# Kernel optimization log

Hardware: AMD Instinct MI355X
Metric: run time of the kernel (lower is better)

Reference implementation:

```python
import jax, jax.numpy as jnp
import numpy as np

B, T, D, H = 2048, 2048, 3, 32  # batch, time steps, input_size, hidden_size


def setup_inputs() -> dict:
    key = jax.random.key(0)
    k0, k1, k2, k3, k4 = jax.random.split(key, 5)
    lim = 1.0 / np.sqrt(H)  # eqx.nn.GRUCell init range
    inp = jax.random.normal(k0, (B, T, D), dtype=jnp.float32)
    weight_ih = jax.random.uniform(k1, (3 * H, D), minval=-lim, maxval=lim, dtype=jnp.float32)
    weight_hh = jax.random.uniform(k2, (3 * H, H), minval=-lim, maxval=lim, dtype=jnp.float32)
    bias = jax.random.uniform(k3, (3 * H,), minval=-lim, maxval=lim, dtype=jnp.float32)
    bias_n = jax.random.uniform(k4, (H,), minval=-lim, maxval=lim, dtype=jnp.float32)
    return {"inp": inp, "weight_ih": weight_ih, "weight_hh": weight_hh,
            "bias": bias, "bias_n": bias_n}


def reference(inp, weight_ih, weight_hh, bias, bias_n):
    # inp: [B, T, D]. Faithful batched version of PinnWithGRU.__call__:
    # scan an eqx.nn.GRUCell over time from a zero hidden state, output hidden[0] per step.
    b = inp.shape[0]
    h0 = jnp.zeros((b, H), dtype=inp.dtype)
    xs = jnp.swapaxes(inp, 0, 1)  # [T, B, D]

    def step(h, x):
        ig = x @ weight_ih.T + bias      # [B, 3H] input gates (+ bias, as in eqx)
        hg = h @ weight_hh.T             # [B, 3H] hidden gates
        ir, iz, ia = jnp.split(ig, 3, axis=-1)
        hr, hz, ha = jnp.split(hg, 3, axis=-1)
        r = jax.nn.sigmoid(ir + hr)
        z = jax.nn.sigmoid(iz + hz)
        n = jnp.tanh(ia + bias_n + r * ha)
        h_new = (1.0 - z) * n + z * h
        return h_new, h_new[:, 0]        # emit first hidden unit per step

    _, out = jax.lax.scan(step, h0, xs)  # out: [T, B]
    return jnp.swapaxes(out, 0, 1)[..., None]  # [B, T, 1] (matches per-seq [T, 1])
```

## Files before the change

### kernel.cpp

```cpp
#include <hip/hip_runtime.h>


#define GRU_B 2048
#define GRU_T 2048
#define GRU_D 3
#define GRU_H 32
#define CHUNK 32
#define XPAD 104

typedef unsigned int uint2v __attribute__((ext_vector_type(2)));

__device__ __forceinline__ float fast_sigmoid(float x) {
    float e = __expf(-x);
    return __builtin_amdgcn_rcpf(1.0f + e);
}
__device__ __forceinline__ float fast_tanh(float x) {
    float e = __expf(2.0f * x);
    return 1.0f - 2.0f * __builtin_amdgcn_rcpf(e + 1.0f);
}

#define DPPF(v, CTRL) __int_as_float(__builtin_amdgcn_update_dpp( \
    0, __float_as_int(v), (CTRL), 0xF, 0xF, false))

template<bool SEL>
__device__ __forceinline__ float swap32(float v) {
    uint2v r = __builtin_amdgcn_permlane32_swap(
        __float_as_uint(v), __float_as_uint(v), false, false);
    return __uint_as_float(SEL ? r.x : r.y);
}

template<bool SEL>
__device__ void gru_fast(
    const float* __restrict__ xp, float* __restrict__ ob,
    const float* __restrict__ w_ih, const float* __restrict__ w_hh,
    const float* __restrict__ bias, const float* __restrict__ bias_n,
    float* __restrict__ x_lds, int lane, int hf, int p, int dir)
{
    const int li = lane & 15;
    const int bb = 16 * (lane >> 5);

    float wrO[16], wrX[16], wzO[16], wzX[16], wnO[16], wnX[16];
#pragma unroll
    for (int j = 0; j < 16; ++j) {
        const int kk = (li + dir * j + 16) & 15;
        const int kown = bb + kk;
        const int koth = (bb ^ 16) + kk;
        wrO[j] = w_hh[(size_t)p * GRU_H + kown];
        wrX[j] = w_hh[(size_t)p * GRU_H + koth];
        wzO[j] = w_hh[(size_t)(GRU_H + p) * GRU_H + kown];
        wzX[j] = w_hh[(size_t)(GRU_H + p) * GRU_H + koth];
        wnO[j] = w_hh[(size_t)(2 * GRU_H + p) * GRU_H + kown];
        wnX[j] = w_hh[(size_t)(2 * GRU_H + p) * GRU_H + koth];
    }
    float wir[GRU_D], wiz[GRU_D], win[GRU_D];
#pragma unroll
    for (int d = 0; d < GRU_D; ++d) {
        wir[d] = w_ih[(size_t)p * GRU_D + d];
        wiz[d] = w_ih[(size_t)(GRU_H + p) * GRU_D + d];
        win[d] = w_ih[(size_t)(2 * GRU_H + p) * GRU_D + d];
    }
    const float bR = bias[p];
    const float bZ = bias[GRU_H + p];
    const float bN = bias[2 * GRU_H + p] + bias_n[p];

    float* xw = x_lds + XPAD * hf;
    const float* xr = x_lds + XPAD * hf;

    float h = 0.0f;
    float xa = xp[p], xb = xp[32 + p], xc = xp[64 + p];

    for (int c = 0; c < GRU_T / CHUNK; ++c) {
        xw[p] = xa; xw[32 + p] = xb; xw[64 + p] = xc;
        if (c + 1 < GRU_T / CHUNK) {
            const size_t nb = (size_t)(c + 1) * (CHUNK * GRU_D);
            xa = xp[nb + p]; xb = xp[nb + 32 + p]; xc = xp[nb + 64 + p];
        }
        float x0c = xr[0], x1c = xr[1], x2c = xr[2];
        float outreg = 0.0f;

#pragma unroll 8
        for (int s = 0; s < CHUNK; ++s) {
            const float aR = fmaf(wir[2], x2c, fmaf(wir[1], x1c, fmaf(wir[0], x0c, bR)));
            const float aZ = fmaf(wiz[2], x2c, fmaf(wiz[1], x1c, fmaf(wiz[0], x0c, bZ)));
            const float aN = fmaf(win[2], x2c, fmaf(win[1], x1c, fmaf(win[0], x0c, bN)));

            float x0n = x0c, x1n = x1c, x2n = x2c;
            if (s + 1 < CHUNK) {
                x0n = xr[3 * (s + 1) + 0];
                x1n = xr[3 * (s + 1) + 1];
                x2n = xr[3 * (s + 1) + 2];
            }

            const float hsw = swap32<SEL>(h);
            float hr_[16], ho_[16];
            hr_[0] = h;    ho_[0] = hsw;
            hr_[1]  = DPPF(h, 0x121);   ho_[1]  = DPPF(hsw, 0x121);
            hr_[2]  = DPPF(h, 0x122);   ho_[2]  = DPPF(hsw, 0x122);
            hr_[3]  = DPPF(h, 0x123);   ho_[3]  = DPPF(hsw, 0x123);
            hr_[4]  = DPPF(h, 0x124);   ho_[4]  = DPPF(hsw, 0x124);
            hr_[5]  = DPPF(h, 0x125);   ho_[5]  = DPPF(hsw, 0x125);
            hr_[6]  = DPPF(h, 0x126);   ho_[6]  = DPPF(hsw, 0x126);
            hr_[7]  = DPPF(h, 0x127);   ho_[7]  = DPPF(hsw, 0x127);
            hr_[8]  = DPPF(h, 0x128);   ho_[8]  = DPPF(hsw, 0x128);
            hr_[9]  = DPPF(h, 0x129);   ho_[9]  = DPPF(hsw, 0x129);
            hr_[10] = DPPF(h, 0x12A);   ho_[10] = DPPF(hsw, 0x12A);
            hr_[11] = DPPF(h, 0x12B);   ho_[11] = DPPF(hsw, 0x12B);
            hr_[12] = DPPF(h, 0x12C);   ho_[12] = DPPF(hsw, 0x12C);
            hr_[13] = DPPF(h, 0x12D);   ho_[13] = DPPF(hsw, 0x12D);
            hr_[14] = DPPF(h, 0x12E);   ho_[14] = DPPF(hsw, 0x12E);
            hr_[15] = DPPF(h, 0x12F);   ho_[15] = DPPF(hsw, 0x12F);

            float rO0 = aR, rO1 = 0.f, rX0 = 0.f, rX1 = 0.f;
            float zO0 = aZ, zO1 = 0.f, zX0 = 0.f, zX1 = 0.f;
            float nO0 = 0.f, nO1 = 0.f, nX0 = 0.f, nX1 = 0.f;
#pragma unroll
            for (int j = 0; j < 8; ++j) {
                rO0 = fmaf(wrO[j],     hr_[j],     rO0);
                rO1 = fmaf(wrO[j + 8], hr_[j + 8], rO1);
                rX0 = fmaf(wrX[j],     ho_[j],     rX0);
                rX1 = fmaf(wrX[j + 8], ho_[j + 8], rX1);
                zO0 = fmaf(wzO[j],     hr_[j],     zO0);
                zO1 = fmaf(wzO[j + 8], hr_[j + 8], zO1);
                zX0 = fmaf(wzX[j],     ho_[j],     zX0);
                zX1 = fmaf(wzX[j + 8], ho_[j + 8], zX1);
                nO0 = fmaf(wnO[j],     hr_[j],     nO0);
                nO1 = fmaf(wnO[j + 8], hr_[j + 8], nO1);
                nX0 = fmaf(wnX[j],     ho_[j],     nX0);
                nX1 = fmaf(wnX[j + 8], ho_[j + 8], nX1);
            }
            const float rs = (rO0 + rO1) + (rX0 + rX1);
            const float zs = (zO0 + zO1) + (zX0 + zX1);
            const float ns = (nO0 + nO1) + (nX0 + nX1);

            const float rg = fast_sigmoid(rs);
            const float zg = fast_sigmoid(zs);
            const float ng = fast_tanh(fmaf(rg, ns, aN));
            h = fmaf(zg, h - ng, ng);

            const float h0A = __uint_as_float(
                (unsigned)__builtin_amdgcn_readfirstlane(__float_as_int(h)));
            const float h0B = __uint_as_float(
                (unsigned)__builtin_amdgcn_readlane(__float_as_int(h), 16));
            const float want = hf ? h0B : h0A;
            if (p == s) outreg = want;

            x0c = x0n; x1c = x1n; x2c = x2n;
        }
        ob[c * CHUNK + p] = outreg;
    }
}

__device__ void gru_lds(
    const float* __restrict__ xp, float* __restrict__ ob,
    const float* __restrict__ w_ih, const float* __restrict__ w_hh,
    const float* __restrict__ bias, const float* __restrict__ bias_n,
    float* __restrict__ x_lds, float* __restrict__ out_stage,
    float* __restrict__ h2, int lane, int hf, int p)
{
    float wr[32], wz[32], wn[32];
#pragma unroll
    for (int k = 0; k < 32; ++k) {
        wr[k] = w_hh[(size_t)p * GRU_H + k];
        wz[k] = w_hh[(size_t)(GRU_H + p) * GRU_H + k];
        wn[k] = w_hh[(size_t)(2 * GRU_H + p) * GRU_H + k];
    }
    float wir[GRU_D], wiz[GRU_D], win[GRU_D];
#pragma unroll
    for (int d = 0; d < GRU_D; ++d) {
        wir[d] = w_ih[(size_t)p * GRU_D + d];
        wiz[d] = w_ih[(size_t)(GRU_H + p) * GRU_D + d];
        win[d] = w_ih[(size_t)(2 * GRU_H + p) * GRU_D + d];
    }
    const float bR = bias[p];
    const float bZ = bias[GRU_H + p];
    const float bN = bias[2 * GRU_H + p] + bias_n[p];

    float* hw = h2 + 48 * hf + p;
    const float4* hv = (const float4*)(h2 + 48 * hf);
    float* xw = x_lds + XPAD * hf;
    const float* xr = x_lds + XPAD * hf;
    float* osw = out_stage + 32 * hf;
    const bool cap = (lane & 47) == 0;

    float h = 0.0f;
    *hw = 0.0f;
    float xa = xp[p], xb = xp[32 + p], xc = xp[64 + p];

    for (int c = 0; c < GRU_T / CHUNK; ++c) {
        xw[p] = xa; xw[32 + p] = xb; xw[64 + p] = xc;
        if (c + 1 < GRU_T / CHUNK) {
            const size_t nb = (size_t)(c + 1) * (CHUNK * GRU_D);
            xa = xp[nb + p]; xb = xp[nb + 32 + p]; xc = xp[nb + 64 + p];
        }
#pragma unroll 8
        for (int s = 0; s < CHUNK; ++s) {
            const float x0 = xr[3 * s + 0];
            const float x1 = xr[3 * s + 1];
            const float x2 = xr[3 * s + 2];
            float4 hk[8];
#pragma unroll
            for (int q = 0; q < 8; ++q) hk[q] = hv[q];

            const float aR = fmaf(wir[2], x2, fmaf(wir[1], x1, fmaf(wir[0], x0, bR)));
            const float aZ = fmaf(wiz[2], x2, fmaf(wiz[1], x1, fmaf(wiz[0], x0, bZ)));
            const float aN = fmaf(win[2], x2, fmaf(win[1], x1, fmaf(win[0], x0, bN)));

            float r0 = aR, r1 = 0.f, z0 = aZ, z1 = 0.f, n0 = 0.f, n1 = 0.f;
#pragma unroll
            for (int q = 0; q < 8; ++q) {
                const float4 v = hk[q];
                r0 = fmaf(wr[4*q+0], v.x, r0); r1 = fmaf(wr[4*q+1], v.y, r1);
                r0 = fmaf(wr[4*q+2], v.z, r0); r1 = fmaf(wr[4*q+3], v.w, r1);
                z0 = fmaf(wz[4*q+0], v.x, z0); z1 = fmaf(wz[4*q+1], v.y, z1);
                z0 = fmaf(wz[4*q+2], v.z, z0); z1 = fmaf(wz[4*q+3], v.w, z1);
                n0 = fmaf(wn[4*q+0], v.x, n0); n1 = fmaf(wn[4*q+1], v.y, n1);
                n0 = fmaf(wn[4*q+2], v.z, n0); n1 = fmaf(wn[4*q+3], v.w, n1);
            }
            const float rg = fast_sigmoid(r0 + r1);
            const float zg = fast_sigmoid(z0 + z1);
            const float ng = fast_tanh(fmaf(rg, n0 + n1, aN));
            h = fmaf(zg, h - ng, ng);
            if (cap) osw[s] = h;
            *hw = h;
        }
        const float ov = osw[p];
        ob[c * CHUNK + p] = ov;
    }
}

__global__ __launch_bounds__(64, 1) void gru_scan_kernel(
    const float* __restrict__ inp, const float* __restrict__ w_ih,
    const float* __restrict__ w_hh, const float* __restrict__ bias,
    const float* __restrict__ bias_n, float* __restrict__ out)
{
    __shared__ __align__(16) float x_lds[2 * XPAD];
    __shared__ __align__(16) float out_stage[2 * CHUNK];
    __shared__ __align__(16) float h2[80];

    const int lane = threadIdx.x;
    const int hf   = (lane >> 4) & 1;
    const int p    = (lane & 15) + 16 * (lane >> 5);
    const size_t seq = 2 * (size_t)blockIdx.x + hf;

    const float* xp = inp + seq * (size_t)(GRU_T * GRU_D);
    float*       ob = out + seq * (size_t)GRU_T;

    int dir = 0;
    bool swapok = false, sel = false;
    {
        const int li = lane & 15;
        const int d1 = __builtin_amdgcn_update_dpp(0, li, 0x121, 0xF, 0xF, false);
        if (__ballot(d1 == ((li + 1) & 15)) == ~0ULL)       dir = 1;
        else if (__ballot(d1 == ((li + 15) & 15)) == ~0ULL) dir = -1;

        const unsigned ul = (unsigned)lane;
        uint2v q = __builtin_amdgcn_permlane32_swap(ul, ul, false, false);
        const unsigned want = ul ^ 32u;
        const bool okA = __ballot(q.x == want) == ~0ULL;
        const bool okB = __ballot(q.y == want) == ~0ULL;
        swapok = okA || okB;
        sel = okA;
    }

    if (dir != 0 && swapok) {
        if (sel) gru_fast<true >(xp, ob, w_ih, w_hh, bias, bias_n,
                                 x_lds, lane, hf, p, dir);
        else     gru_fast<false>(xp, ob, w_ih, w_hh, bias, bias_n,
                                 x_lds, lane, hf, p, dir);
    } else {
        gru_lds(xp, ob, w_ih, w_hh, bias, bias_n,
                x_lds, out_stage, h2, lane, hf, p);
    }
}

extern "C" void kernel_launch(void* const* d_in, const int* in_sizes, int n_in,
                              void* d_out, int out_size, void* d_ws, size_t ws_size,
                              hipStream_t stream) {
    const float* inp    = (const float*)d_in[0];
    const float* w_ih   = (const float*)d_in[1];
    const float* w_hh   = (const float*)d_in[2];
    const float* bias   = (const float*)d_in[3];
    const float* bias_n = (const float*)d_in[4];
    float* out = (float*)d_out;

    dim3 grid(GRU_B / 2);
    dim3 block(64);
    gru_scan_kernel<<<grid, block, 0, stream>>>(inp, w_ih, w_hh, bias, bias_n, out);
}
```

Baseline: 601.2 us.

## Fuse DPP rotations into fmac instructions and re-layout hidden state exchange

Replaces the separate DPP row-rotate moves plus FMA loop with inline-asm v_fmac_f32_dpp chains, so each rotation is folded into the multiply-accumulate. It also changes how hidden state is distributed across lanes: after each step, the upper half-wave's copy of h is exchanged via permlane16_swap (or ds_bpermute as a fallback), and the previous-state value is selected per lane. This aims to cut instruction count and latency on the serial recurrence critical path. The trade-offs are that each accumulator is now a single serial dependency chain instead of several independent partial sums, and an extra cross-lane exchange is added per step.

After: 616.9 us. 2.6% more time.

```diff
diff --git a/kernel.cpp b/kernel.cpp
--- a/kernel.cpp
+++ b/kernel.cpp
@@ -18,9 +18,9 @@
     float e = __expf(2.0f * x);
     return 1.0f - 2.0f * __builtin_amdgcn_rcpf(e + 1.0f);
 }
-
-#define DPPF(v, CTRL) __int_as_float(__builtin_amdgcn_update_dpp( \
-    0, __float_as_int(v), (CTRL), 0xF, 0xF, false))
+__device__ __forceinline__ float bperm(float v, int baddr) {
+    return __int_as_float(__builtin_amdgcn_ds_bpermute(baddr, __float_as_int(v)));
+}
 
 template<bool SEL>
 __device__ __forceinline__ float swap32(float v) {
@@ -29,12 +29,43 @@
     return __uint_as_float(SEL ? r.x : r.y);
 }
 
-template<bool SEL>
+#if __has_builtin(__builtin_amdgcn_permlane16_swap)
+#define HAVE_P16 1
+#else
+#define HAVE_P16 0
+#endif
+
+#define DOT16(ACC, HSRC, W) \
+  asm("s_nop 1\n\t" \
+      "v_fmac_f32 %0, %1, %2\n\t" \
+      "v_fmac_f32_dpp %0, %1, %3 row_ror:1 row_mask:0xf bank_mask:0xf\n\t" \
+      "v_fmac_f32_dpp %0, %1, %4 row_ror:2 row_mask:0xf bank_mask:0xf\n\t" \
+      "v_fmac_f32_dpp %0, %1, %5 row_ror:3 row_mask:0xf bank_mask:0xf\n\t" \
+      "v_fmac_f32_dpp %0, %1, %6 row_ror:4 row_mask:0xf bank_mask:0xf\n\t" \
+      "v_fmac_f32_dpp %0, %1, %7 row_ror:5 row_mask:0xf bank_mask:0xf\n\t" \
+      "v_fmac_f32_dpp %0, %1, %8 row_ror:6 row_mask:0xf bank_mask:0xf\n\t" \
+      "v_fmac_f32_dpp %0, %1, %9 row_ror:7 row_mask:0xf bank_mask:0xf\n\t" \
+      "v_fmac_f32_dpp %0, %1, %10 row_ror:8 row_mask:0xf bank_mask:0xf\n\t" \
+      "v_fmac_f32_dpp %0, %1, %11 row_ror:9 row_mask:0xf bank_mask:0xf\n\t" \
+      "v_fmac_f32_dpp %0, %1, %12 row_ror:10 row_mask:0xf bank_mask:0xf\n\t" \
+      "v_fmac_f32_dpp %0, %1, %13 row_ror:11 row_mask:0xf bank_mask:0xf\n\t" \
+      "v_fmac_f32_dpp %0, %1, %14 row_ror:12 row_mask:0xf bank_mask:0xf\n\t" \
+      "v_fmac_f32_dpp %0, %1, %15 row_ror:13 row_mask:0xf bank_mask:0xf\n\t" \
+      "v_fmac_f32_dpp %0, %1, %16 row_ror:14 row_mask:0xf bank_mask:0xf\n\t" \
+      "v_fmac_f32_dpp %0, %1, %17 row_ror:15 row_mask:0xf bank_mask:0xf" \
+      : "+v"(ACC) \
+      : "v"(HSRC), "v"((W)[0]), "v"((W)[1]), "v"((W)[2]), "v"((W)[3]), \
+        "v"((W)[4]), "v"((W)[5]), "v"((W)[6]), "v"((W)[7]), "v"((W)[8]), \
+        "v"((W)[9]), "v"((W)[10]), "v"((W)[11]), "v"((W)[12]), "v"((W)[13]), \
+        "v"((W)[14]), "v"((W)[15]))
+
+template<bool SEL32, bool USE16>
 __device__ void gru_fast(
     const float* __restrict__ xp, float* __restrict__ ob,
     const float* __restrict__ w_ih, const float* __restrict__ w_hh,
     const float* __restrict__ bias, const float* __restrict__ bias_n,
-    float* __restrict__ x_lds, int lane, int hf, int p, int dir)
+    float* __restrict__ x_lds, int lane, int hf, int p, int dir,
+    bool sel16, int a16)
 {
     const int li = lane & 15;
     const int bb = 16 * (lane >> 5);
@@ -91,58 +122,48 @@
                 x2n = xr[3 * (s + 1) + 2];
             }
 
-            const float hsw = swap32<SEL>(h);
-            float hr_[16], ho_[16];
-            hr_[0] = h;    ho_[0] = hsw;
-            hr_[1]  = DPPF(h, 0x121);   ho_[1]  = DPPF(hsw, 0x121);
-            hr_[2]  = DPPF(h, 0x122);   ho_[2]  = DPPF(hsw, 0x122);
-            hr_[3]  = DPPF(h, 0x123);   ho_[3]  = DPPF(hsw, 0x123);
-            hr_[4]  = DPPF(h, 0x124);   ho_[4]  = DPPF(hsw, 0x124);
-            hr_[5]  = DPPF(h, 0x125);   ho_[5]  = DPPF(hsw, 0x125);
-            hr_[6]  = DPPF(h, 0x126);   ho_[6]  = DPPF(hsw, 0x126);
-            hr_[7]  = DPPF(h, 0x127);   ho_[7]  = DPPF(hsw, 0x127);
-            hr_[8]  = DPPF(h, 0x128);   ho_[8]  = DPPF(hsw, 0x128);
-            hr_[9]  = DPPF(h, 0x129);   ho_[9]  = DPPF(hsw, 0x129);
-            hr_[10] = DPPF(h, 0x12A);   ho_[10] = DPPF(hsw, 0x12A);
-            hr_[11] = DPPF(h, 0x12B);   ho_[11] = DPPF(hsw, 0x12B);
-            hr_[12] = DPPF(h, 0x12C);   ho_[12] = DPPF(hsw, 0x12C);
-            hr_[13] = DPPF(h, 0x12D);   ho_[13] = DPPF(hsw, 0x12D);
-            hr_[14] = DPPF(h, 0x12E);   ho_[14] = DPPF(hsw, 0x12E);
-            hr_[15] = DPPF(h, 0x12F);   ho_[15] = DPPF(hsw, 0x12F);
-
-            float rO0 = aR, rO1 = 0.f, rX0 = 0.f, rX1 = 0.f;
-            float zO0 = aZ, zO1 = 0.f, zX0 = 0.f, zX1 = 0.f;
-            float nO0 = 0.f, nO1 = 0.f, nX0 = 0.f, nX1 = 0.f;
-#pragma unroll
-            for (int j = 0; j < 8; ++j) {
-                rO0 = fmaf(wrO[j],     hr_[j],     rO0);
-                rO1 = fmaf(wrO[j + 8], hr_[j + 8], rO1);
-                rX0 = fmaf(wrX[j],     ho_[j],     rX0);
-                rX1 = fmaf(wrX[j + 8], ho_[j + 8], rX1);
-                zO0 = fmaf(wzO[j],     hr_[j],     zO0);
-                zO1 = fmaf(wzO[j + 8], hr_[j + 8], zO1);
-                zX0 = fmaf(wzX[j],     ho_[j],     zX0);
-                zX1 = fmaf(wzX[j + 8], ho_[j + 8], zX1);
-                nO0 = fmaf(wnO[j],     hr_[j],     nO0);
-                nO1 = fmaf(wnO[j + 8], hr_[j + 8], nO1);
-                nX0 = fmaf(wnX[j],     ho_[j],     nX0);
-                nX1 = fmaf(wnX[j + 8], ho_[j + 8], nX1);
-            }
-            const float rs = (rO0 + rO1) + (rX0 + rX1);
-            const float zs = (zO0 + zO1) + (zX0 + zX1);
-            const float ns = (nO0 + nO1) + (nX0 + nX1);
+            const float hsw = swap32<SEL32>(h);
+            const float hprev = (lane & 32) ? hsw : h;
+
+            float accOr = aR,  accXr = 0.0f;
+            float accOz = aZ,  accXz = 0.0f;
+            float accOn = 0.f, accXn = 0.0f;
+            DOT16(accOr, h,   wrO);
+            DOT16(accXr, hsw, wrX);
+            DOT16(accOz, h,   wzO);
+            DOT16(accXz, hsw, wzX);
+            DOT16(accOn, h,   wnO);
+            DOT16(accXn, hsw, wnX);
+
+            const float rs = accOr + accXr;
+            const float zs = accOz + accXz;
+            const float ns = accOn + accXn;
 
             const float rg = fast_sigmoid(rs);
             const float zg = fast_sigmoid(zs);
             const float ng = fast_tanh(fmaf(rg, ns, aN));
-            h = fmaf(zg, h - ng, ng);
+            const float hnew = fmaf(zg, hprev - ng, ng);
 
             const float h0A = __uint_as_float(
-                (unsigned)__builtin_amdgcn_readfirstlane(__float_as_int(h)));
+                (unsigned)__builtin_amdgcn_readfirstlane(__float_as_int(hnew)));
             const float h0B = __uint_as_float(
-                (unsigned)__builtin_amdgcn_readlane(__float_as_int(h), 16));
+                (unsigned)__builtin_amdgcn_readlane(__float_as_int(hnew), 16));
             const float want = hf ? h0B : h0A;
             if (p == s) outreg = want;
+
+            float fv;
+            if constexpr (USE16) {
+#if HAVE_P16
+                uint2v f = __builtin_amdgcn_permlane16_swap(
+                    __float_as_uint(hnew), __float_as_uint(hnew), false, false);
+                fv = __uint_as_float(sel16 ? f.x : f.y);
+#else
+                fv = bperm(hnew, a16);
+#endif
+            } else {
+                fv = bperm(hnew, a16);
+            }
+            h = (lane & 32) ? fv : hnew;
 
             x0c = x0n; x1c = x1n; x2c = x2n;
         }
@@ -244,9 +265,10 @@
 
     const float* xp = inp + seq * (size_t)(GRU_T * GRU_D);
     float*       ob = out + seq * (size_t)GRU_T;
+    const int a16 = (lane ^ 16) << 2;
 
     int dir = 0;
-    bool swapok = false, sel = false;
+    bool ok32 = false, sel32 = false, ok16 = false, sel16 = false;
     {
         const int li = lane & 15;
         const int d1 = __builtin_amdgcn_update_dpp(0, li, 0x121, 0xF, 0xF, false);
@@ -255,18 +277,32 @@
 
         const unsigned ul = (unsigned)lane;
         uint2v q = __builtin_amdgcn_permlane32_swap(ul, ul, false, false);
-        const unsigned want = ul ^ 32u;
-        const bool okA = __ballot(q.x == want) == ~0ULL;
-        const bool okB = __ballot(q.y == want) == ~0ULL;
-        swapok = okA || okB;
-        sel = okA;
-    }
-
-    if (dir != 0 && swapok) {
-        if (sel) gru_fast<true >(xp, ob, w_ih, w_hh, bias, bias_n,
-                                 x_lds, lane, hf, p, dir);
-        else     gru_fast<false>(xp, ob, w_ih, w_hh, bias, bias_n,
-                                 x_lds, lane, hf, p, dir);
+        const unsigned w32 = ul ^ 32u;
+        const bool a = __ballot(q.x == w32) == ~0ULL;
+        const bool b = __ballot(q.y == w32) == ~0ULL;
+        ok32 = a || b; sel32 = a;
+
+#if HAVE_P16
+        uint2v q16 = __builtin_amdgcn_permlane16_swap(ul, ul, false, false);
+        const unsigned w16 = ul ^ 16u;
+        const bool a16ok = __ballot(q16.x == w16) == ~0ULL;
+        const bool b16ok = __ballot(q16.y == w16) == ~0ULL;
+        ok16 = a16ok || b16ok; sel16 = a16ok;
+#endif
+    }
+
+    if (dir != 0 && ok32) {
+        if (ok16) {
+            if (sel32) gru_fast<true,  true >(xp, ob, w_ih, w_hh, bias, bias_n,
+                                              x_lds, lane, hf, p, dir, sel16, a16);
+            else       gru_fast<false, true >(xp, ob, w_ih, w_hh, bias, bias_n,
+                                              x_lds, lane, hf, p, dir, sel16, a16);
+        } else {
+            if (sel32) gru_fast<true,  false>(xp, ob, w_ih, w_hh, bias, bias_n,
+                                              x_lds, lane, hf, p, dir, sel16, a16);
+            else       gru_fast<false, false>(xp, ob, w_ih, w_hh, bias, bias_n,
+                                              x_lds, lane, hf, p, dir, sel16, a16);
+        }
     } else {
         gru_lds(xp, ob, w_ih, w_hh, bias, bias_n,
                 x_lds, out_stage, h2, lane, hf, p);
```
